# Performance work log

Hardware: AMD Instinct MI355X
Metric: run time of the kernel (lower is better)

Reference implementation:

```python
import jax, jax.numpy as jnp
import numpy as np

B, N, P, PL = 8, 16, 128, 16
D, DS, DTR, DFF, EL = 128, 16, 8, 256, 2


def setup_inputs() -> dict:
    key = jax.random.key(0)
    ks = jax.random.split(key, 16)
    g = lambda i, shape, s=0.02: jax.random.normal(ks[i], shape, dtype=jnp.float32) * s
    A_init = jnp.broadcast_to(jnp.log(jnp.arange(1, DS + 1, dtype=jnp.float32)), (EL, 2, D, DS))
    return dict(
        x=jax.random.normal(ks[0], (B, N, P, PL), dtype=jnp.float32),
        view=jax.random.normal(ks[1], (B, 1, D), dtype=jnp.float32),
        wp_w=g(2, (D, PL)), wp_b=jnp.zeros((D,), jnp.float32),
        m_in_w=g(3, (EL, 2, 2 * D, D)),
        m_conv_w=g(4, (EL, 2, D, 2), 0.5), m_conv_b=jnp.zeros((EL, 2, D), jnp.float32),
        m_xproj_w=g(5, (EL, 2, DTR + 2 * DS, D)),
        m_dt_w=g(6, (EL, 2, D, DTR), 0.1), m_dt_b=jnp.full((EL, 2, D), -4.6, jnp.float32),
        m_Alog=jnp.array(A_init),
        m_D=jnp.ones((EL, 2, D), jnp.float32),
        m_out_w=g(7, (EL, 2, D, D)),
        ffn_w1=g(8, (EL, DFF, D)), ffn_b1=jnp.zeros((EL, DFF), jnp.float32),
        ffn_w2=g(9, (EL, D, DFF)), ffn_b2=jnp.zeros((EL, D), jnp.float32),
        ln1_g=jnp.ones((EL, D), jnp.float32), ln1_b=jnp.zeros((EL, D), jnp.float32),
        ln2_g=jnp.ones((EL, D), jnp.float32), ln2_b=jnp.zeros((EL, D), jnp.float32),
        lnf_g=jnp.ones((D,), jnp.float32), lnf_b=jnp.zeros((D,), jnp.float32),
    )


def _ln(x, g, b, eps=1e-5):
    m = x.mean(-1, keepdims=True)
    v = x.var(-1, keepdims=True)
    return (x - m) * jax.lax.rsqrt(v + eps) * g + b


def _mamba(u, in_w, conv_w, conv_b, xproj_w, dt_w, dt_b, A_log, Dp, out_w):
    # u: [b, L, d]; d_inner == d_model (expand=1), causal depthwise conv with kernel 2
    dtr, ds = dt_w.shape[1], A_log.shape[1]
    xz = u @ in_w.T                               # [b, L, 2d]
    xc, z = jnp.split(xz, 2, axis=-1)
    xp = jnp.pad(xc, ((0, 0), (1, 0), (0, 0)))    # left-pad (d_conv-1 = 1)
    xc = xp[:, :-1, :] * conv_w[:, 0] + xp[:, 1:, :] * conv_w[:, 1] + conv_b
    xc = jax.nn.silu(xc)
    dbc = xc @ xproj_w.T                          # [b, L, dtr + 2*ds]
    dt = jax.nn.softplus(dbc[..., :dtr] @ dt_w.T + dt_b)   # [b, L, d]
    Bm = dbc[..., dtr:dtr + ds]                   # [b, L, n]
    Cm = dbc[..., dtr + ds:]                      # [b, L, n]
    A = -jnp.exp(A_log)                           # [d, n]
    dA = jnp.exp(dt[..., None] * A)               # [b, L, d, n]
    dBx = dt[..., None] * Bm[:, :, None, :] * xc[..., None]  # [b, L, d, n]

    def step(h, ab):
        a, bx = ab
        h = a * h + bx
        return h, h

    h0 = jnp.zeros((u.shape[0], dt.shape[-1], ds), u.dtype)
    _, hs = jax.lax.scan(step, h0, (jnp.moveaxis(dA, 1, 0), jnp.moveaxis(dBx, 1, 0)))
    y = jnp.einsum('lbdn,bln->bld', hs, Cm)       # [b, L, d]
    y = y + xc * Dp
    y = y * jax.nn.silu(z)
    return y @ out_w.T


def _layer(u, pf, pr, w1, b1, w2, b2, g1, be1, g2, be2):
    fwd = _mamba(u, *pf)
    rev = _mamba(u[:, ::-1], *pr)[:, ::-1]
    u = u + fwd + rev
    xr = _ln(u, g1, be1)
    y = jax.nn.relu(xr @ w1.T + b1) @ w2.T + b2   # 1x1 conv FFN == pointwise linear
    return _ln(xr + y, g2, be2)


def reference(x, view, wp_w, wp_b, m_in_w, m_conv_w, m_conv_b, m_xproj_w, m_dt_w,
              m_dt_b, m_Alog, m_D, m_out_w, ffn_w1, ffn_b1, ffn_w2, ffn_b2,
              ln1_g, ln1_b, ln2_g, ln2_b, lnf_g, lnf_b):
    b, n, p, _ = x.shape
    u = x @ wp_w.T + wp_b                         # [b, n, p, d]
    d = u.shape[-1]
    u = u.reshape(b, n * p, d)
    u = jnp.concatenate([u, view], axis=1)        # [b, n*p+1, d]
    for l in range(m_in_w.shape[0]):
        pf = (m_in_w[l, 0], m_conv_w[l, 0], m_conv_b[l, 0], m_xproj_w[l, 0],
              m_dt_w[l, 0], m_dt_b[l, 0], m_Alog[l, 0], m_D[l, 0], m_out_w[l, 0])
        pr = (m_in_w[l, 1], m_conv_w[l, 1], m_conv_b[l, 1], m_xproj_w[l, 1],
              m_dt_w[l, 1], m_dt_b[l, 1], m_Alog[l, 1], m_D[l, 1], m_out_w[l, 1])
        u = _layer(u, pf, pr, ffn_w1[l], ffn_b1[l], ffn_w2[l], ffn_b2[l],
                   ln1_g[l], ln1_b[l], ln2_g[l], ln2_b[l])
    u = _ln(u, lnf_g, lnf_b)
    z = u[:, :-1, :].reshape(b, n, p, d)
    return z.transpose(0, 1, 3, 2)                # [b, n, d, p]
```

## Files before the change

kernel.cpp:

```cpp
#include <hip/hip_runtime.h>
#include <hip/hip_bf16.h>
#include <math.h>

#define DEV __device__ __forceinline__

constexpr int B  = 8,  N = 16, P = 128, PL = 16;
constexpr int D  = 128, DS = 16, DTR = 8, DFF = 256, EL = 2;
constexpr int L  = N * P + 1;
constexpr int BL = B * L;
constexpr int CT = 32;
constexpr int NC = (L + CT - 1) / CT;
constexpr int MT64  = (BL + 63) / 64;
constexpr int KS = 136;
constexpr int HS = 264;

using bf16x8 = __attribute__((ext_vector_type(8))) __bf16;
using f32x4  = __attribute__((ext_vector_type(4))) float;

DEV float sigmoidf_(float x) { return 1.0f / (1.0f + __expf(-x)); }

DEV void pow_tree(float r, float* pw) {
  float r2 = r * r;
  float r3 = r2 * r;
  float r4 = r2 * r2;
  float r8 = r4 * r4;
  float r12 = r8 * r4;
  pw[0] = r;       pw[1] = r2;      pw[2] = r3;      pw[3] = r4;
  pw[4] = r4 * r;  pw[5] = r4 * r2; pw[6] = r4 * r3; pw[7] = r8;
  pw[8] = r8 * r;  pw[9] = r8 * r2; pw[10] = r8 * r3; pw[11] = r12;
  pw[12] = r12 * r; pw[13] = r12 * r2; pw[14] = r12 * r3; pw[15] = r12 * r4;
}

DEV bool an_is_linear(const float* An) {
  bool ok = true;
#pragma unroll
  for (int n = 0; n < DS; ++n)
    ok = ok && (fabsf(An[n] + (float)(n + 1)) < 1e-3f * (n + 1));
  return ok;
}

__global__ __launch_bounds__(256) void k_prep(
    const float* __restrict__ in_w, const float* __restrict__ conv_w,
    const float* __restrict__ xproj, const float* __restrict__ out_w,
    const float* __restrict__ w1, const float* __restrict__ w2,
    __bf16* __restrict__ weff, __bf16* __restrict__ xpw_bf,
    __bf16* __restrict__ outw_bf, __bf16* __restrict__ w1_bf,
    __bf16* __restrict__ w2_bf)
{
  int g = blockIdx.x * 256 + threadIdx.x;
  if (g < 262144) {
    int l = g >> 17;
    int r = g & 131071;
    int dir = r >> 16;
    int r2 = r & 65535;
    int col = r2 >> 8;
    int kk = r2 & 255;
    int chunk = kk >> 7, k = kk & 127;
    int ld = l * 2 + dir;
    float v;
    if (col < 128) {
      v = in_w[((size_t)ld * 256 + col) * 128 + k] *
          conv_w[((size_t)ld * 128 + col) * 2 + chunk];
    } else {
      v = chunk ? in_w[((size_t)ld * 256 + col) * 128 + k] : 0.f;
    }
    weff[((size_t)ld * 256 + col) * 256 + chunk * 128 + k] = (__bf16)v;
    return;
  }
  g -= 262144;
  if (g < 20480) { xpw_bf[g] = (__bf16)xproj[g]; return; }
  g -= 20480;
  if (g < 65536) {
    int k = g & 127; int q = g >> 7; int n = q & 127; int q2 = q >> 7;
    int dir = q2 & 1; int l = q2 >> 1;
    outw_bf[((size_t)(l * 128 + n)) * 256 + dir * 128 + k] = (__bf16)out_w[g];
    return;
  }
  g -= 65536;
  if (g < 65536) { w1_bf[g] = (__bf16)w1[g]; return; }
  g -= 65536;
  if (g < 65536) { w2_bf[g] = (__bf16)w2[g]; return; }
}

__global__ __launch_bounds__(256) void k_embed(
    const float* __restrict__ x, const float* __restrict__ view,
    const float* __restrict__ wp_w, const float* __restrict__ wp_b,
    float* __restrict__ U, __bf16* __restrict__ Ubf)
{
  int g = blockIdx.x * 256 + threadIdx.x;
  if (g >= BL * D) return;
  int d = g & (D - 1);
  int row = g >> 7;
  int b = row / L, t = row % L;
  float acc;
  if (t < N * P) {
    const float* xr = x + ((size_t)b * N * P + t) * PL;
    acc = wp_b[d];
#pragma unroll
    for (int k = 0; k < PL; ++k) acc += xr[k] * wp_w[d * PL + k];
  } else {
    acc = view[b * D + d];
  }
  U[(size_t)row * D + d] = acc;
  Ubf[(size_t)row * D + d] = (__bf16)acc;
}

__global__ __launch_bounds__(256) void k_front(
    const __bf16* __restrict__ Ubf, const __bf16* __restrict__ Weff,
    const float* __restrict__ conv_b_l, const __bf16* __restrict__ xpw,
    const float* __restrict__ dt_w_l, const float* __restrict__ dt_b_l,
    __bf16* __restrict__ XCCbf, __bf16* __restrict__ Zbf,
    float* __restrict__ BCb, __bf16* __restrict__ DTbf)
{
  __shared__ short As[64 * KS];
  __shared__ short Ws[64 * KS];
  __shared__ float dbs[64][9];
  int bx = blockIdx.x;
  int rdir = bx / MT64;
  int tile = bx % MT64;
  bool isx = (blockIdx.y == 0);
  int tid = threadIdx.x;
  int m0 = tile * 64;
  const __bf16* Wb = Weff + (size_t)rdir * 256 * 256;
  int wave = tid >> 6, lane = tid & 63, lm = lane & 15, lq = lane >> 4;
  int rr0 = tid >> 4, gcol = tid & 15;

  int aoff[4];
  unsigned vmask = 0, smask = 0;
  int shif = rdir ? 128 : -128;
#pragma unroll
  for (int i = 0; i < 4; ++i) {
    int rr = rr0 + 16 * i;
    int m = m0 + rr;
    aoff[i] = 0;
    if (m < BL) {
      int b = m / L, s = m - b * L;
      int idx1 = rdir ? (L - 1 - s) : s;
      aoff[i] = (b * L + idx1) * 128 + gcol * 8;
      vmask |= 1u << i;
      if (s >= 1) smask |= 1u << i;
    }
  }

  f32x4 zero4 = {0.f, 0.f, 0.f, 0.f};
  f32x4 acc[8];
#pragma unroll
  for (int c = 0; c < 8; ++c) acc[c] = zero4;

  int kc0 = isx ? 0 : 1;
  int colx = isx ? 0 : 128;
  for (int kc = kc0; kc < 2; ++kc) {
    if (kc != kc0) __syncthreads();
    {
      int4 av[4];
#pragma unroll
      for (int i = 0; i < 4; ++i) {
        av[i] = make_int4(0, 0, 0, 0);
        bool ok = (vmask >> i) & 1;
        if (kc == 0) ok = ok && ((smask >> i) & 1);
        if (ok) av[i] = *(const int4*)(Ubf + aoff[i] + (kc == 0 ? shif : 0));
      }
#pragma unroll
      for (int i = 0; i < 4; ++i)
        *(int4*)&As[(rr0 + 16 * i) * KS + gcol * 8] = av[i];
    }
    for (int ch = 0; ch < 2; ++ch) {
      if (ch) __syncthreads();
      {
        int4 wv[4];
#pragma unroll
        for (int i = 0; i < 4; ++i)
          wv[i] = *(const int4*)(Wb + (size_t)(colx + ch * 64 + rr0 + 16 * i) * 256 + kc * 128 + gcol * 8);
#pragma unroll
        for (int i = 0; i < 4; ++i)
          *(int4*)&Ws[(rr0 + 16 * i) * KS + gcol * 8] = wv[i];
      }
      __syncthreads();
      for (int ks = 0; ks < 128; ks += 32) {
        bf16x8 af = *(const bf16x8*)&As[(wave * 16 + lm) * KS + ks + lq * 8];
#pragma unroll
        for (int c = 0; c < 4; ++c) {
          bf16x8 bfr = *(const bf16x8*)&Ws[(c * 16 + lm) * KS + ks + lq * 8];
          acc[ch * 4 + c] = __builtin_amdgcn_mfma_f32_16x16x32_bf16(af, bfr, acc[ch * 4 + c], 0, 0, 0);
        }
      }
    }
  }

  if (!isx) {
#pragma unroll
    for (int cg = 0; cg < 8; ++cg) {
      int col = cg * 16 + lm;
#pragma unroll
      for (int e = 0; e < 4; ++e) {
        int m = m0 + wave * 16 + lq * 4 + e;
        if (m < BL)
          Zbf[((size_t)rdir * BL + m) * 128 + col] = (__bf16)acc[cg][e];
      }
    }
    return;
  }

  __syncthreads();
#pragma unroll
  for (int cg = 0; cg < 8; ++cg) {
    int col = cg * 16 + lm;
    float cb = conv_b_l[rdir * 128 + col];
#pragma unroll
    for (int e = 0; e < 4; ++e) {
      int rl = wave * 16 + lq * 4 + e;
      int m = m0 + rl;
      float v = acc[cg][e] + cb;
      float o = v * sigmoidf_(v);
      __bf16 ob = (__bf16)o;
      if (m < BL) XCCbf[((size_t)rdir * BL + m) * 128 + col] = ob;
      As[rl * KS + col] = (short)__builtin_bit_cast(unsigned short, ob);
    }
  }
  {
    int4 xv[3];
#pragma unroll
    for (int i = 0; i < 3; ++i) {
      int rr = rr0 + 16 * i;
      xv[i] = make_int4(0, 0, 0, 0);
      if (rr < 40) xv[i] = *(const int4*)(xpw + ((size_t)rdir * 40 + rr) * 128 + gcol * 8);
    }
#pragma unroll
    for (int i = 0; i < 3; ++i)
      *(int4*)&Ws[(rr0 + 16 * i) * KS + gcol * 8] = xv[i];
  }
  __syncthreads();
  f32x4 acc2[3];
#pragma unroll
  for (int c = 0; c < 3; ++c) acc2[c] = zero4;
  for (int ks = 0; ks < 128; ks += 32) {
    bf16x8 af = *(const bf16x8*)&As[(wave * 16 + lm) * KS + ks + lq * 8];
#pragma unroll
    for (int c = 0; c < 3; ++c) {
      bf16x8 bfr = *(const bf16x8*)&Ws[(c * 16 + lm) * KS + ks + lq * 8];
      acc2[c] = __builtin_amdgcn_mfma_f32_16x16x32_bf16(af, bfr, acc2[c], 0, 0, 0);
    }
  }
#pragma unroll
  for (int c = 0; c < 3; ++c) {
    int col = c * 16 + lm;
#pragma unroll
    for (int e = 0; e < 4; ++e) {
      int rl = wave * 16 + lq * 4 + e;
      int m = m0 + rl;
      float v = acc2[c][e];
      if (col < DTR) dbs[rl][col] = v;
      else if (col < DTR + 2 * DS && m < BL)
        BCb[((size_t)rdir * BL + m) * 32 + (col - DTR)] = v;
    }
  }
  __syncthreads();
  {
    int dloc = tid & 127;
    int rpar = tid >> 7;
    const float* dw = dt_w_l + ((size_t)rdir * 128 + dloc) * 8;
    float dwr[8];
#pragma unroll
    for (int j = 0; j < 8; ++j) dwr[j] = dw[j];
    float db = dt_b_l[rdir * 128 + dloc];
    for (int rr = rpar; rr < 64; rr += 2) {
      int m = m0 + rr;
      if (m >= BL) break;
      float a = db;
#pragma unroll
      for (int j = 0; j < 8; ++j) a = fmaf(dbs[rr][j], dwr[j], a);
      float dtv = (a > 20.f) ? a : log1pf(__expf(a));
      DTbf[((size_t)rdir * BL + m) * 128 + dloc] = (__bf16)dtv;
    }
  }
}

__global__ __launch_bounds__(128) void k_scanA(
    const __bf16* __restrict__ DTbf, const __bf16* __restrict__ XCCbf,
    const float* __restrict__ BCb, const float* __restrict__ Alog_l,
    float* __restrict__ HC, float* __restrict__ DTS)
{
  __shared__ float Bs[CT][DS];
  __shared__ __bf16 DTs[CT][128];
  __shared__ __bf16 XCs[CT][128];
  __shared__ float HT[128][DS + 1];
  int blk = blockIdx.x;
  int c  = blk % NC;
  int rb = blk / NC;
  int rdir = rb / B;
  int d = threadIdx.x;
  int s0 = c * CT;
  int cn = min(CT, L - s0);
  size_t rowbase = (size_t)rb * L + s0;

  int totB = cn * DS;
  float bb[4]; bool bp[4];
#pragma unroll
  for (int i = 0; i < 4; ++i) {
    int q = d + i * 128;
    bp[i] = q < totB;
    bb[i] = bp[i] ? BCb[(rowbase + (q >> 4)) * 32 + (q & 15)] : 0.f;
  }
  int totD = cn * 16;
  int4 dv[4], xv[4]; bool dp[4];
#pragma unroll
  for (int i = 0; i < 4; ++i) {
    int q = d + i * 128;
    dp[i] = q < totD;
    dv[i] = make_int4(0, 0, 0, 0);
    xv[i] = make_int4(0, 0, 0, 0);
    int row = q >> 4, c8 = (q & 15) * 8;
    if (dp[i]) {
      dv[i] = *(const int4*)(DTbf + (rowbase + row) * D + c8);
      xv[i] = *(const int4*)(XCCbf + (rowbase + row) * D + c8);
    }
  }
  float An[DS];
  const float* Ab = Alog_l + (size_t)rdir * D * DS + (size_t)d * DS;
#pragma unroll
  for (int n = 0; n < DS; ++n) An[n] = -__expf(Ab[n]);
  bool fast = an_is_linear(An);
#pragma unroll
  for (int i = 0; i < 4; ++i) {
    int q = d + i * 128;
    if (bp[i]) Bs[q >> 4][q & 15] = bb[i];
  }
#pragma unroll
  for (int i = 0; i < 4; ++i) {
    int q = d + i * 128;
    int row = q >> 4, c8 = (q & 15) * 8;
    if (dp[i]) {
      *(int4*)&DTs[row][c8] = dv[i];
      *(int4*)&XCs[row][c8] = xv[i];
    }
  }
  __syncthreads();
  float h[DS];
#pragma unroll
  for (int n = 0; n < DS; ++n) h[n] = 0.f;
  float dts = 0.f;
  if (fast) {
    for (int ss = 0; ss < cn; ++ss) {
      float dt = (float)DTs[ss][d];
      float xc = (float)XCs[ss][d];
      dts += dt;
      float e = dt * xc;
      float pw[DS];
      pow_tree(__expf(-dt), pw);
#pragma unroll
      for (int n = 0; n < DS; ++n)
        h[n] = fmaf(pw[n], h[n], e * Bs[ss][n]);
    }
  } else {
    for (int ss = 0; ss < cn; ++ss) {
      float dt = (float)DTs[ss][d];
      float xc = (float)XCs[ss][d];
      dts += dt;
      float e = dt * xc;
#pragma unroll
      for (int n = 0; n < DS; ++n)
        h[n] = __expf(dt * An[n]) * h[n] + e * Bs[ss][n];
    }
  }
  DTS[(size_t)blk * D + d] = dts;
#pragma unroll
  for (int n = 0; n < DS; ++n) HT[d][n] = h[n];
  __syncthreads();
  for (int q = d; q < D * DS; q += 128) {
    int n = q >> 7, dd = q & 127;
    HC[((size_t)blk * DS + n) * D + dd] = HT[dd][n];
  }
}

__global__ __launch_bounds__(128) void k_scanB(
    const float* __restrict__ HC, const float* __restrict__ DTS,
    const float* __restrict__ Alog_l, float* __restrict__ HIN)
{
  int rb = blockIdx.x >> 4;
  int n  = blockIdx.x & 15;
  int rdir = rb / B;
  int d = threadIdx.x;
  float An_v = -__expf(Alog_l[((size_t)rdir * D + d) * DS + n]);
  float hc[8], dts[8];
#pragma unroll
  for (int k = 0; k < 8; ++k) {
    int cc = (k < NC) ? k : NC - 1;
    hc[k]  = HC[((size_t)(rb * NC + cc) * DS + n) * D + d];
    dts[k] = DTS[((size_t)(rb * NC + cc)) * D + d];
  }
  float h = 0.f;
  for (int c = 0; c < NC; c += 8) {
#pragma unroll
    for (int k = 0; k < 8; ++k) {
      int cc = c + k;
      if (cc >= NC) break;
      HIN[((size_t)(rb * NC + cc) * DS + n) * D + d] = h;
      h = __expf(dts[k] * An_v) * h + hc[k];
      int cp = cc + 8 < NC ? cc + 8 : NC - 1;
      hc[k]  = HC[((size_t)(rb * NC + cp) * DS + n) * D + d];
      dts[k] = DTS[((size_t)(rb * NC + cp)) * D + d];
    }
  }
}

__global__ __launch_bounds__(128) void k_scanC(
    const __bf16* __restrict__ DTbf, const __bf16* __restrict__ XCCbf,
    const float* __restrict__ BCb, const __bf16* __restrict__ Zbf,
    const float* __restrict__ HIN, const float* __restrict__ Alog_l,
    const float* __restrict__ Dp_l, __bf16* __restrict__ YMbf)
{
  __shared__ float Bsm[CT][DS];
  __shared__ float Csm[CT][DS];
  __shared__ __bf16 DTs[CT][128];
  __shared__ __bf16 XCs[CT][128];
  __shared__ __bf16 Zs[CT][128];
  int blk = blockIdx.x;
  int c  = blk % NC;
  int rb = blk / NC;
  int rdir = rb / B;
  int b = rb % B;
  int d = threadIdx.x;
  int s0 = c * CT;
  int cn = min(CT, L - s0);
  size_t rowbase = (size_t)rb * L + s0;

  int tot2 = cn * 2 * DS;
  float cbv[8]; bool cbp[8];
#pragma unroll
  for (int i = 0; i < 8; ++i) {
    int q = d + i * 128;
    cbp[i] = q < tot2;
    cbv[i] = cbp[i] ? BCb[(rowbase + (q >> 5)) * 32 + (q & 31)] : 0.f;
  }
  int totD = cn * 16;
  int4 dv[4], xv[4], zv[4]; bool dp[4];
#pragma unroll
  for (int i = 0; i < 4; ++i) {
    int q = d + i * 128;
    dp[i] = q < totD;
    dv[i] = make_int4(0, 0, 0, 0);
    xv[i] = make_int4(0, 0, 0, 0);
    zv[i] = make_int4(0, 0, 0, 0);
    int row = q >> 4, c8 = (q & 15) * 8;
    if (dp[i]) {
      dv[i] = *(const int4*)(DTbf + (rowbase + row) * D + c8);
      xv[i] = *(const int4*)(XCCbf + (rowbase + row) * D + c8);
      zv[i] = *(const int4*)(Zbf + (rowbase + row) * D + c8);
    }
  }
  float An[DS];
  const float* Ab = Alog_l + (size_t)rdir * D * DS + (size_t)d * DS;
#pragma unroll
  for (int n = 0; n < DS; ++n) An[n] = -__expf(Ab[n]);
  bool fast = an_is_linear(An);
  float h[DS];
#pragma unroll
  for (int n = 0; n < DS; ++n)
    h[n] = HIN[((size_t)blk * DS + n) * D + d];
  float Dpv = Dp_l[rdir * D + d];
#pragma unroll
  for (int i = 0; i < 8; ++i) {
    int q = d + i * 128;
    if (cbp[i]) {
      int ss = q >> 5, j = q & 31;
      if (j < DS) Bsm[ss][j] = cbv[i]; else Csm[ss][j - DS] = cbv[i];
    }
  }
#pragma unroll
  for (int i = 0; i < 4; ++i) {
    int q = d + i * 128;
    int row = q >> 4, c8 = (q & 15) * 8;
    if (dp[i]) {
      *(int4*)&DTs[row][c8] = dv[i];
      *(int4*)&XCs[row][c8] = xv[i];
      *(int4*)&Zs[row][c8]  = zv[i];
    }
  }
  __syncthreads();
  if (fast) {
    for (int ss = 0; ss < cn; ++ss) {
      float dt = (float)DTs[ss][d];
      float xc = (float)XCs[ss][d];
      float z  = (float)Zs[ss][d];
      float e = dt * xc;
      float pw[DS];
      pow_tree(__expf(-dt), pw);
      float y = xc * Dpv;
#pragma unroll
      for (int n = 0; n < DS; ++n) {
        h[n] = fmaf(pw[n], h[n], e * Bsm[ss][n]);
        y = fmaf(h[n], Csm[ss][n], y);
      }
      y *= z * sigmoidf_(z);
      int s = s0 + ss;
      int tt = rdir ? (L - 1 - s) : s;
      YMbf[((size_t)b * L + tt) * 256 + rdir * 128 + d] = (__bf16)y;
    }
  } else {
    for (int ss = 0; ss < cn; ++ss) {
      float dt = (float)DTs[ss][d];
      float xc = (float)XCs[ss][d];
      float z  = (float)Zs[ss][d];
      float e = dt * xc;
      float y = xc * Dpv;
#pragma unroll
      for (int n = 0; n < DS; ++n) {
        h[n] = __expf(dt * An[n]) * h[n] + e * Bsm[ss][n];
        y = fmaf(h[n], Csm[ss][n], y);
      }
      y *= z * sigmoidf_(z);
      int s = s0 + ss;
      int tt = rdir ? (L - 1 - s) : s;
      YMbf[((size_t)b * L + tt) * 256 + rdir * 128 + d] = (__bf16)y;
    }
  }
}

__global__ __launch_bounds__(256) void k_tail(
    const __bf16* __restrict__ YMbf, const __bf16* __restrict__ Wout,
    const float* __restrict__ g1, const float* __restrict__ be1,
    const __bf16* __restrict__ w1bf, const float* __restrict__ b1,
    const __bf16* __restrict__ w2bf, const float* __restrict__ b2,
    const float* __restrict__ g2, const float* __restrict__ be2,
    float* __restrict__ U, __bf16* __restrict__ Ubf,
    int last, const float* __restrict__ lnfg, const float* __restrict__ lnfb,
    float* __restrict__ outp)
{
  __shared__ short AX[64 * KS];
  __shared__ short BH[128 * KS];
  __shared__ short Ws[64 * KS];
  int m0 = blockIdx.x * 64;
  int tid = threadIdx.x;
  int wave = tid >> 6, lane = tid & 63, lm = lane & 15, lq = lane >> 4;
  int rr0 = tid >> 4, gcol = tid & 15;
  f32x4 zero4 = {0.f, 0.f, 0.f, 0.f};

  float uvp[4][8];
#pragma unroll
  for (int r = 0; r < 4; ++r) {
    int row = m0 + wave * 16 + lq * 4 + r;
    bool valid = row < BL;
#pragma unroll
    for (int c = 0; c < 8; ++c) {
      int col = c * 16 + lm;
      uvp[r][c] = valid ? U[(size_t)row * 128 + col] : 0.f;
    }
  }

  int4 w1v0[4], w1v1[4], w1v2[4], w1v3[4];
  f32x4 acc[8];
#pragma unroll
  for (int c = 0; c < 8; ++c) acc[c] = zero4;
#pragma unroll
  for (int kc = 0; kc < 2; ++kc) {
    if (kc) __syncthreads();
    {
      int4 ymv[4];
#pragma unroll
      for (int j = 0; j < 4; ++j) {
        int m = m0 + rr0 + j * 16;
        ymv[j] = make_int4(0, 0, 0, 0);
        if (m < BL) ymv[j] = *(const int4*)(YMbf + (size_t)m * 256 + kc * 128 + gcol * 8);
      }
      int4 wov[8];
#pragma unroll
      for (int j = 0; j < 8; ++j)
        wov[j] = *(const int4*)(Wout + (size_t)(rr0 + j * 16) * 256 + kc * 128 + gcol * 8);
#pragma unroll
      for (int j = 0; j < 4; ++j)
        *(int4*)&AX[(rr0 + j * 16) * KS + gcol * 8] = ymv[j];
#pragma unroll
      for (int j = 0; j < 8; ++j)
        *(int4*)&BH[(rr0 + j * 16) * KS + gcol * 8] = wov[j];
    }
    if (kc == 1) {
#pragma unroll
      for (int j = 0; j < 4; ++j)
        w1v0[j] = *(const int4*)(w1bf + (size_t)(0 * 64 + rr0 + j * 16) * 128 + gcol * 8);
#pragma unroll
      for (int j = 0; j < 4; ++j)
        w1v1[j] = *(const int4*)(w1bf + (size_t)(1 * 64 + rr0 + j * 16) * 128 + gcol * 8);
#pragma unroll
      for (int j = 0; j < 4; ++j)
        w1v2[j] = *(const int4*)(w1bf + (size_t)(2 * 64 + rr0 + j * 16) * 128 + gcol * 8);
#pragma unroll
      for (int j = 0; j < 4; ++j)
        w1v3[j] = *(const int4*)(w1bf + (size_t)(3 * 64 + rr0 + j * 16) * 128 + gcol * 8);
    }
    __syncthreads();
    for (int ks = 0; ks < 128; ks += 32) {
      bf16x8 af = *(const bf16x8*)&AX[(wave * 16 + lm) * KS + ks + lq * 8];
#pragma unroll
      for (int c = 0; c < 8; ++c) {
        bf16x8 bfr = *(const bf16x8*)&BH[(c * 16 + lm) * KS + ks + lq * 8];
        acc[c] = __builtin_amdgcn_mfma_f32_16x16x32_bf16(af, bfr, acc[c], 0, 0, 0);
      }
    }
  }
  __syncthreads();

  {
    float g1c[8], be1c[8];
#pragma unroll
    for (int c = 0; c < 8; ++c) {
      int col = c * 16 + lm;
      g1c[c] = g1[col]; be1c[c] = be1[col];
    }
#pragma unroll
    for (int r = 0; r < 4; ++r) {
      float os[8];
      float sum = 0.f;
#pragma unroll
      for (int c = 0; c < 8; ++c) {
        os[c] = acc[c][r] + uvp[r][c];
        sum += os[c];
      }
#pragma unroll
      for (int mm = 1; mm < 16; mm <<= 1) sum += __shfl_xor(sum, mm, 64);
      float mean = sum * (1.f / 128.f);
      float qv = 0.f;
#pragma unroll
      for (int c = 0; c < 8; ++c) { float dv = os[c] - mean; qv += dv * dv; }
#pragma unroll
      for (int mm = 1; mm < 16; mm <<= 1) qv += __shfl_xor(qv, mm, 64);
      float inv = rsqrtf(qv * (1.f / 128.f) + 1e-5f);
      int rl = wave * 16 + lq * 4 + r;
#pragma unroll
      for (int c = 0; c < 8; ++c) {
        int col = c * 16 + lm;
        float o = (os[c] - mean) * inv * g1c[c] + be1c[c];
        AX[rl * KS + col] = (short)__builtin_bit_cast(unsigned short, (__bf16)o);
      }
    }
  }

  int4 w2v0[4], w2v1[4], w2v2[4], w2v3[4];
#pragma unroll
  for (int cc = 0; cc < 4; ++cc) {
    __syncthreads();
#pragma unroll
    for (int j = 0; j < 4; ++j) {
      int4 wv = (cc == 0) ? w1v0[j] : (cc == 1) ? w1v1[j] : (cc == 2) ? w1v2[j] : w1v3[j];
      *(int4*)&Ws[(rr0 + j * 16) * KS + gcol * 8] = wv;
    }
    if (cc == 3) {
#pragma unroll
      for (int j = 0; j < 4; ++j)
        w2v0[j] = *(const int4*)(w2bf + (size_t)(0 * 64 + rr0 + j * 16) * 256 + 0 * 128 + gcol * 8);
#pragma unroll
      for (int j = 0; j < 4; ++j)
        w2v1[j] = *(const int4*)(w2bf + (size_t)(0 * 64 + rr0 + j * 16) * 256 + 1 * 128 + gcol * 8);
#pragma unroll
      for (int j = 0; j < 4; ++j)
        w2v2[j] = *(const int4*)(w2bf + (size_t)(1 * 64 + rr0 + j * 16) * 256 + 0 * 128 + gcol * 8);
#pragma unroll
      for (int j = 0; j < 4; ++j)
        w2v3[j] = *(const int4*)(w2bf + (size_t)(1 * 64 + rr0 + j * 16) * 256 + 1 * 128 + gcol * 8);
    }
    __syncthreads();
    f32x4 a1[4];
#pragma unroll
    for (int c = 0; c < 4; ++c) a1[c] = zero4;
    for (int ks = 0; ks < 128; ks += 32) {
      bf16x8 af = *(const bf16x8*)&AX[(wave * 16 + lm) * KS + ks + lq * 8];
#pragma unroll
      for (int c = 0; c < 4; ++c) {
        bf16x8 bfr = *(const bf16x8*)&Ws[(c * 16 + lm) * KS + ks + lq * 8];
        a1[c] = __builtin_amdgcn_mfma_f32_16x16x32_bf16(af, bfr, a1[c], 0, 0, 0);
      }
    }
#pragma unroll
    for (int c = 0; c < 4; ++c) {
      int col = cc * 64 + c * 16 + lm;
      float bb = b1[col];
#pragma unroll
      for (int e = 0; e < 4; ++e) {
        int rl = wave * 16 + lq * 4 + e;
        float hv = fmaxf(a1[c][e] + bb, 0.f);
        BH[rl * HS + col] = (short)__builtin_bit_cast(unsigned short, (__bf16)hv);
      }
    }
  }

  f32x4 a2[2][4];
#pragma unroll
  for (int nc = 0; nc < 2; ++nc)
#pragma unroll
    for (int c = 0; c < 4; ++c) a2[nc][c] = zero4;
#pragma unroll
  for (int ph = 0; ph < 4; ++ph) {
    int nc = ph >> 1, kc = ph & 1;
    __syncthreads();
#pragma unroll
    for (int j = 0; j < 4; ++j) {
      int4 wv = (ph == 0) ? w2v0[j] : (ph == 1) ? w2v1[j] : (ph == 2) ? w2v2[j] : w2v3[j];
      *(int4*)&Ws[(rr0 + j * 16) * KS + gcol * 8] = wv;
    }
    __syncthreads();
    for (int ks = 0; ks < 128; ks += 32) {
      bf16x8 af = *(const bf16x8*)&BH[(wave * 16 + lm) * HS + kc * 128 + ks + lq * 8];
#pragma unroll
      for (int c = 0; c < 4; ++c) {
        bf16x8 bfr = *(const bf16x8*)&Ws[(c * 16 + lm) * KS + ks + lq * 8];
        a2[nc][c] = __builtin_amdgcn_mfma_f32_16x16x32_bf16(af, bfr, a2[nc][c], 0, 0, 0);
      }
    }
  }
  {
    float b2c[8], g2c[8], be2c[8];
#pragma unroll
    for (int q = 0; q < 8; ++q) {
      int col = (q >> 2) * 64 + (q & 3) * 16 + lm;
      b2c[q] = b2[col]; g2c[q] = g2[col]; be2c[q] = be2[col];
    }
#pragma unroll
    for (int r = 0; r < 4; ++r) {
      int rl = wave * 16 + lq * 4 + r;
      int row = m0 + rl;
      bool valid = row < BL;
      float os[8];
      float sum = 0.f;
#pragma unroll
      for (int q = 0; q < 8; ++q) {
        int nc = q >> 2, c = q & 3;
        int col = nc * 64 + c * 16 + lm;
        __bf16 xb = __builtin_bit_cast(__bf16, (unsigned short)AX[rl * KS + col]);
        os[q] = a2[nc][c][r] + b2c[q] + (float)xb;
        sum += os[q];
      }
#pragma unroll
      for (int mm = 1; mm < 16; mm <<= 1) sum += __shfl_xor(sum, mm, 64);
      float mean = sum * (1.f / 128.f);
      float qv = 0.f;
#pragma unroll
      for (int q = 0; q < 8; ++q) { float dv = os[q] - mean; qv += dv * dv; }
#pragma unroll
      for (int mm = 1; mm < 16; mm <<= 1) qv += __shfl_xor(qv, mm, 64);
      float inv = rsqrtf(qv * (1.f / 128.f) + 1e-5f);
      float o[8];
#pragma unroll
      for (int q = 0; q < 8; ++q)
        o[q] = (os[q] - mean) * inv * g2c[q] + be2c[q];
      if (!last) {
        if (valid) {
#pragma unroll
          for (int q = 0; q < 8; ++q) {
            int col = (q >> 2) * 64 + (q & 3) * 16 + lm;
            U[(size_t)row * 128 + col] = o[q];
          }
        }
#pragma unroll
        for (int q = 0; q < 8; ++q) {
          int col = (q >> 2) * 64 + (q & 3) * 16 + lm;
          AX[rl * KS + col] = (short)__builtin_bit_cast(unsigned short, (__bf16)o[q]);
        }
      } else {
        float s2 = 0.f;
#pragma unroll
        for (int q = 0; q < 8; ++q) s2 += o[q];
#pragma unroll
        for (int mm = 1; mm < 16; mm <<= 1) s2 += __shfl_xor(s2, mm, 64);
        float mean2 = s2 * (1.f / 128.f);
        float qv2 = 0.f;
#pragma unroll
        for (int q = 0; q < 8; ++q) { float dv = o[q] - mean2; qv2 += dv * dv; }
#pragma unroll
        for (int mm = 1; mm < 16; mm <<= 1) qv2 += __shfl_xor(qv2, mm, 64);
        float inv2 = rsqrtf(qv2 * (1.f / 128.f) + 1e-5f);
        if (valid) {
          int bb = row / L;
          int t = row - bb * L;
          if (t < N * P) {
            int n = t >> 7, p = t & 127;
            size_t obase = (((size_t)bb * N + n) * D) * P + p;
#pragma unroll
            for (int q = 0; q < 8; ++q) {
              int col = (q >> 2) * 64 + (q & 3) * 16 + lm;
              float o2 = (o[q] - mean2) * inv2 * lnfg[col] + lnfb[col];
              outp[obase + (size_t)col * P] = o2;
            }
          }
        }
      }
    }
  }
  if (!last) {
    __syncthreads();
#pragma unroll
    for (int i = 0; i < 4; ++i) {
      int rr = rr0 + 16 * i;
      int m = m0 + rr;
      if (m < BL)
        *(int4*)(Ubf + (size_t)m * 128 + gcol * 8) = *(const int4*)&AX[rr * KS + gcol * 8];
    }
  }
}

extern "C" void kernel_launch(void* const* d_in, const int* in_sizes, int n_in,
                              void* d_out, int out_size, void* d_ws, size_t ws_size,
                              hipStream_t stream)
{
  (void)in_sizes; (void)n_in; (void)out_size; (void)ws_size;
  const float* x       = (const float*)d_in[0];
  const float* view    = (const float*)d_in[1];
  const float* wp_w    = (const float*)d_in[2];
  const float* wp_b    = (const float*)d_in[3];
  const float* m_in_w  = (const float*)d_in[4];
  const float* m_conv_w= (const float*)d_in[5];
  const float* m_conv_b= (const float*)d_in[6];
  const float* m_xproj = (const float*)d_in[7];
  const float* m_dt_w  = (const float*)d_in[8];
  const float* m_dt_b  = (const float*)d_in[9];
  const float* m_Alog  = (const float*)d_in[10];
  const float* m_Dp    = (const float*)d_in[11];
  const float* m_out_w = (const float*)d_in[12];
  const float* ffn_w1  = (const float*)d_in[13];
  const float* ffn_b1  = (const float*)d_in[14];
  const float* ffn_w2  = (const float*)d_in[15];
  const float* ffn_b2  = (const float*)d_in[16];
  const float* ln1_g   = (const float*)d_in[17];
  const float* ln1_b   = (const float*)d_in[18];
  const float* ln2_g   = (const float*)d_in[19];
  const float* ln2_b   = (const float*)d_in[20];
  const float* lnf_g   = (const float*)d_in[21];
  const float* lnf_b   = (const float*)d_in[22];
  float* out = (float*)d_out;

  float* W = (float*)d_ws;
  size_t off = 0;
  auto alloc = [&](size_t nfl) { float* p = W + off; off += (nfl + 3) & ~(size_t)3; return p; };
  float* U      = alloc((size_t)BL * D);
  float* Ubf_f  = alloc((size_t)BL * D / 2);
  float* XCC_f  = alloc((size_t)BL * D);
  float* Zbf_f  = alloc((size_t)BL * D);
  float* DT_f   = alloc((size_t)BL * D);
  float* BCb    = alloc((size_t)2 * BL * 2 * DS);
  float* YM_f   = alloc((size_t)BL * 256 / 2);
  float* HC     = alloc((size_t)2 * B * NC * D * DS);
  float* DTS    = alloc((size_t)2 * B * NC * D);
  float* HIN    = alloc((size_t)2 * B * NC * D * DS);
  float* weff_f = alloc(262144 / 2);
  float* xpw_f  = alloc(20480 / 2);
  float* outw_f = alloc(65536 / 2);
  float* w1_f   = alloc(65536 / 2);
  float* w2_f   = alloc(65536 / 2);

  __bf16* Ubf    = (__bf16*)Ubf_f;
  __bf16* XCCbf  = (__bf16*)XCC_f;
  __bf16* Zbf    = (__bf16*)Zbf_f;
  __bf16* DTbf   = (__bf16*)DT_f;
  __bf16* YMbf   = (__bf16*)YM_f;
  __bf16* weff   = (__bf16*)weff_f;
  __bf16* xpw_bf = (__bf16*)xpw_f;
  __bf16* outw_bf= (__bf16*)outw_f;
  __bf16* w1_bf  = (__bf16*)w1_f;
  __bf16* w2_bf  = (__bf16*)w2_f;

  k_prep<<<1872, 256, 0, stream>>>(m_in_w, m_conv_w, m_xproj, m_out_w, ffn_w1, ffn_w2,
                                   weff, xpw_bf, outw_bf, w1_bf, w2_bf);
  k_embed<<<(BL * D + 255) / 256, 256, 0, stream>>>(x, view, wp_w, wp_b, U, Ubf);

  for (int l = 0; l < EL; ++l) {
    const float* conv_b_l = m_conv_b + (size_t)l * 2 * D;
    const float* dt_w_l   = m_dt_w   + (size_t)l * 2 * D * DTR;
    const float* dt_b_l   = m_dt_b   + (size_t)l * 2 * D;
    const float* Alog_l   = m_Alog   + (size_t)l * 2 * D * DS;
    const float* Dp_l     = m_Dp     + (size_t)l * 2 * D;

    k_front <<<dim3(2 * MT64, 2), 256, 0, stream>>>(
        Ubf, weff + (size_t)l * 2 * 256 * 256, conv_b_l,
        xpw_bf + (size_t)l * 2 * 40 * 128, dt_w_l, dt_b_l,
        XCCbf, Zbf, BCb, DTbf);
    k_scanA <<<2 * B * NC, 128, 0, stream>>>(DTbf, XCCbf, BCb, Alog_l, HC, DTS);
    k_scanB <<<2 * B * 16, 128, 0, stream>>>(HC, DTS, Alog_l, HIN);
    k_scanC <<<2 * B * NC, 128, 0, stream>>>(DTbf, XCCbf, BCb, Zbf, HIN, Alog_l, Dp_l, YMbf);
    k_tail  <<<MT64, 256, 0, stream>>>(
        YMbf, outw_bf + (size_t)l * 128 * 256,
        ln1_g + l * D, ln1_b + l * D,
        w1_bf + (size_t)l * 256 * 128, ffn_b1 + l * DFF,
        w2_bf + (size_t)l * 128 * 256, ffn_b2 + l * D,
        ln2_g + l * D, ln2_b + l * D, U, Ubf,
        (l == EL - 1) ? 1 : 0, lnf_g, lnf_b, out);
  }
}
```

Baseline: 303.5 us.

## Fold inter-chunk scan into scanC and merge prep/embed kernels

Removes the separate k_scanB kernel: each scanC block now recomputes its own incoming chunk state by sequentially combining all preceding chunk summaries (HC, DTS) itself, eliminating the HIN buffer and one launch per layer. The weight-prep and embedding kernels are also merged into a single launch. The trade-off is redundant work: block c reads and combines c chunk summaries (up to about 64), so total reads grow quadratically in chunk count and later chunks take longer, which may create imbalance.

```diff
diff --git a/kernel.cpp b/kernel.cpp
--- a/kernel.cpp
+++ b/kernel.cpp
@@ -13,6 +13,8 @@
 constexpr int MT64  = (BL + 63) / 64;
 constexpr int KS = 136;
 constexpr int HS = 264;
+constexpr int PREP_BLOCKS  = 1872;
+constexpr int EMBED_BLOCKS = (BL * D + 255) / 256;
 
 using bf16x8 = __attribute__((ext_vector_type(8))) __bf16;
 using f32x4  = __attribute__((ext_vector_type(4))) float;
@@ -39,55 +41,55 @@
   return ok;
 }
 
-__global__ __launch_bounds__(256) void k_prep(
+__global__ __launch_bounds__(256) void k_init(
     const float* __restrict__ in_w, const float* __restrict__ conv_w,
     const float* __restrict__ xproj, const float* __restrict__ out_w,
     const float* __restrict__ w1, const float* __restrict__ w2,
     __bf16* __restrict__ weff, __bf16* __restrict__ xpw_bf,
     __bf16* __restrict__ outw_bf, __bf16* __restrict__ w1_bf,
-    __bf16* __restrict__ w2_bf)
-{
-  int g = blockIdx.x * 256 + threadIdx.x;
-  if (g < 262144) {
-    int l = g >> 17;
-    int r = g & 131071;
-    int dir = r >> 16;
-    int r2 = r & 65535;
-    int col = r2 >> 8;
-    int kk = r2 & 255;
-    int chunk = kk >> 7, k = kk & 127;
-    int ld = l * 2 + dir;
-    float v;
-    if (col < 128) {
-      v = in_w[((size_t)ld * 256 + col) * 128 + k] *
-          conv_w[((size_t)ld * 128 + col) * 2 + chunk];
-    } else {
-      v = chunk ? in_w[((size_t)ld * 256 + col) * 128 + k] : 0.f;
-    }
-    weff[((size_t)ld * 256 + col) * 256 + chunk * 128 + k] = (__bf16)v;
-    return;
-  }
-  g -= 262144;
-  if (g < 20480) { xpw_bf[g] = (__bf16)xproj[g]; return; }
-  g -= 20480;
-  if (g < 65536) {
-    int k = g & 127; int q = g >> 7; int n = q & 127; int q2 = q >> 7;
-    int dir = q2 & 1; int l = q2 >> 1;
-    outw_bf[((size_t)(l * 128 + n)) * 256 + dir * 128 + k] = (__bf16)out_w[g];
-    return;
-  }
-  g -= 65536;
-  if (g < 65536) { w1_bf[g] = (__bf16)w1[g]; return; }
-  g -= 65536;
-  if (g < 65536) { w2_bf[g] = (__bf16)w2[g]; return; }
-}
-
-__global__ __launch_bounds__(256) void k_embed(
+    __bf16* __restrict__ w2_bf,
     const float* __restrict__ x, const float* __restrict__ view,
     const float* __restrict__ wp_w, const float* __restrict__ wp_b,
     float* __restrict__ U, __bf16* __restrict__ Ubf)
 {
-  int g = blockIdx.x * 256 + threadIdx.x;
+  int bid = blockIdx.x;
+  if (bid < PREP_BLOCKS) {
+    int g = bid * 256 + threadIdx.x;
+    if (g < 262144) {
+      int l = g >> 17;
+      int r = g & 131071;
+      int dir = r >> 16;
+      int r2 = r & 65535;
+      int col = r2 >> 8;
+      int kk = r2 & 255;
+      int chunk = kk >> 7, k = kk & 127;
+      int ld = l * 2 + dir;
+      float v;
+      if (col < 128) {
+        v = in_w[((size_t)ld * 256 + col) * 128 + k] *
+            conv_w[((size_t)ld * 128 + col) * 2 + chunk];
+      } else {
+        v = chunk ? in_w[((size_t)ld * 256 + col) * 128 + k] : 0.f;
+      }
+      weff[((size_t)ld * 256 + col) * 256 + chunk * 128 + k] = (__bf16)v;
+      return;
+    }
+    g -= 262144;
+    if (g < 20480) { xpw_bf[g] = (__bf16)xproj[g]; return; }
+    g -= 20480;
+    if (g < 65536) {
+      int k = g & 127; int q = g >> 7; int n = q & 127; int q2 = q >> 7;
+      int dir = q2 & 1; int l = q2 >> 1;
+      outw_bf[((size_t)(l * 128 + n)) * 256 + dir * 128 + k] = (__bf16)out_w[g];
+      return;
+    }
+    g -= 65536;
+    if (g < 65536) { w1_bf[g] = (__bf16)w1[g]; return; }
+    g -= 65536;
+    if (g < 65536) { w2_bf[g] = (__bf16)w2[g]; return; }
+    return;
+  }
+  int g = (bid - PREP_BLOCKS) * 256 + threadIdx.x;
   if (g >= BL * D) return;
   int d = g & (D - 1);
   int row = g >> 7;
@@ -372,41 +374,11 @@
   }
 }
 
-__global__ __launch_bounds__(128) void k_scanB(
-    const float* __restrict__ HC, const float* __restrict__ DTS,
-    const float* __restrict__ Alog_l, float* __restrict__ HIN)
-{
-  int rb = blockIdx.x >> 4;
-  int n  = blockIdx.x & 15;
-  int rdir = rb / B;
-  int d = threadIdx.x;
-  float An_v = -__expf(Alog_l[((size_t)rdir * D + d) * DS + n]);
-  float hc[8], dts[8];
-#pragma unroll
-  for (int k = 0; k < 8; ++k) {
-    int cc = (k < NC) ? k : NC - 1;
-    hc[k]  = HC[((size_t)(rb * NC + cc) * DS + n) * D + d];
-    dts[k] = DTS[((size_t)(rb * NC + cc)) * D + d];
-  }
-  float h = 0.f;
-  for (int c = 0; c < NC; c += 8) {
-#pragma unroll
-    for (int k = 0; k < 8; ++k) {
-      int cc = c + k;
-      if (cc >= NC) break;
-      HIN[((size_t)(rb * NC + cc) * DS + n) * D + d] = h;
-      h = __expf(dts[k] * An_v) * h + hc[k];
-      int cp = cc + 8 < NC ? cc + 8 : NC - 1;
-      hc[k]  = HC[((size_t)(rb * NC + cp) * DS + n) * D + d];
-      dts[k] = DTS[((size_t)(rb * NC + cp)) * D + d];
-    }
-  }
-}
-
 __global__ __launch_bounds__(128) void k_scanC(
     const __bf16* __restrict__ DTbf, const __bf16* __restrict__ XCCbf,
     const float* __restrict__ BCb, const __bf16* __restrict__ Zbf,
-    const float* __restrict__ HIN, const float* __restrict__ Alog_l,
+    const float* __restrict__ HC, const float* __restrict__ DTS,
+    const float* __restrict__ Alog_l,
     const float* __restrict__ Dp_l, __bf16* __restrict__ YMbf)
 {
   __shared__ float Bsm[CT][DS];
@@ -453,10 +425,6 @@
 #pragma unroll
   for (int n = 0; n < DS; ++n) An[n] = -__expf(Ab[n]);
   bool fast = an_is_linear(An);
-  float h[DS];
-#pragma unroll
-  for (int n = 0; n < DS; ++n)
-    h[n] = HIN[((size_t)blk * DS + n) * D + d];
   float Dpv = Dp_l[rdir * D + d];
 #pragma unroll
   for (int i = 0; i < 8; ++i) {
@@ -474,6 +442,52 @@
       *(int4*)&DTs[row][c8] = dv[i];
       *(int4*)&XCs[row][c8] = xv[i];
       *(int4*)&Zs[row][c8]  = zv[i];
+    }
+  }
+
+  float h[DS];
+#pragma unroll
+  for (int n = 0; n < DS; ++n) h[n] = 0.f;
+  {
+    const float* HCrb  = HC  + ((size_t)(rb * NC) * DS) * D + d;
+    const float* DTSrb = DTS + (size_t)(rb * NC) * D + d;
+    float dts_c = (c > 0) ? DTSrb[0] : 0.f;
+    float hcv[DS];
+#pragma unroll
+    for (int n = 0; n < DS; ++n)
+      hcv[n] = (c > 0) ? HCrb[(size_t)n * D] : 0.f;
+    if (fast) {
+      for (int cc = 0; cc < c; ++cc) {
+        bool more = (cc + 1) < c;
+        float dts_n = more ? DTSrb[(size_t)(cc + 1) * D] : 0.f;
+        float hn[DS];
+#pragma unroll
+        for (int n = 0; n < DS; ++n)
+          hn[n] = more ? HCrb[((size_t)(cc + 1) * DS + n) * D] : 0.f;
+        float pw[DS];
+        pow_tree(__expf(-dts_c), pw);
+#pragma unroll
+        for (int n = 0; n < DS; ++n)
+          h[n] = fmaf(pw[n], h[n], hcv[n]);
+        dts_c = dts_n;
+#pragma unroll
+        for (int n = 0; n < DS; ++n) hcv[n] = hn[n];
+      }
+    } else {
+      for (int cc = 0; cc < c; ++cc) {
+        bool more = (cc + 1) < c;
+        float dts_n = more ? DTSrb[(size_t)(cc + 1) * D] : 0.f;
+        float hn[DS];
+#pragma unroll
+        for (int n = 0; n < DS; ++n)
+          hn[n] = more ? HCrb[((size_t)(cc + 1) * DS + n) * D] : 0.f;
+#pragma unroll
+        for (int n = 0; n < DS; ++n)
+          h[n] = __expf(dts_c * An[n]) * h[n] + hcv[n];
+        dts_c = dts_n;
+#pragma unroll
+        for (int n = 0; n < DS; ++n) hcv[n] = hn[n];
+      }
     }
   }
   __syncthreads();
@@ -838,7 +852,6 @@
   float* YM_f   = alloc((size_t)BL * 256 / 2);
   float* HC     = alloc((size_t)2 * B * NC * D * DS);
   float* DTS    = alloc((size_t)2 * B * NC * D);
-  float* HIN    = alloc((size_t)2 * B * NC * D * DS);
   float* weff_f = alloc(262144 / 2);
   float* xpw_f  = alloc(20480 / 2);
   float* outw_f = alloc(65536 / 2);
@@ -856,9 +869,10 @@
   __bf16* w1_bf  = (__bf16*)w1_f;
   __bf16* w2_bf  = (__bf16*)w2_f;
 
-  k_prep<<<1872, 256, 0, stream>>>(m_in_w, m_conv_w, m_xproj, m_out_w, ffn_w1, ffn_w2,
-                                   weff, xpw_bf, outw_bf, w1_bf, w2_bf);
-  k_embed<<<(BL * D + 255) / 256, 256, 0, stream>>>(x, view, wp_w, wp_b, U, Ubf);
+  k_init<<<PREP_BLOCKS + EMBED_BLOCKS, 256, 0, stream>>>(
+      m_in_w, m_conv_w, m_xproj, m_out_w, ffn_w1, ffn_w2,
+      weff, xpw_bf, outw_bf, w1_bf, w2_bf,
+      x, view, wp_w, wp_b, U, Ubf);
 
   for (int l = 0; l < EL; ++l) {
     const float* conv_b_l = m_conv_b + (size_t)l * 2 * D;
@@ -872,8 +886,7 @@
         xpw_bf + (size_t)l * 2 * 40 * 128, dt_w_l, dt_b_l,
         XCCbf, Zbf, BCb, DTbf);
     k_scanA <<<2 * B * NC, 128, 0, stream>>>(DTbf, XCCbf, BCb, Alog_l, HC, DTS);
-    k_scanB <<<2 * B * 16, 128, 0, stream>>>(HC, DTS, Alog_l, HIN);
-    k_scanC <<<2 * B * NC, 128, 0, stream>>>(DTbf, XCCbf, BCb, Zbf, HIN, Alog_l, Dp_l, YMbf);
+    k_scanC <<<2 * B * NC, 128, 0, stream>>>(DTbf, XCCbf, BCb, Zbf, HC, DTS, Alog_l, Dp_l, YMbf);
     k_tail  <<<MT64, 256, 0, stream>>>(
         YMbf, outw_bf + (size_t)l * 128 * 256,
         ln1_g + l * D, ln1_b + l * D,
```

After: 366.1 us. 1.21x slower.
